# Performance work log

Measured on AMD Instinct MI355X. Metric: run time of the kernel, lower is better.

The kernel has to match this reference:

```python
import jax, jax.numpy as jnp
import numpy as np

E = 20000      # num edges
S = 64         # mul of 0e (scalar) channels
V = 32         # mul of 1o (vector) channels
FC_IN = 128    # radial basis length
HID = 64       # fc hidden width
INV_SQRT3 = 0.5773502691896258  # CG(1o x 1o -> 0e) = delta_ij / sqrt(3)


def setup_inputs() -> dict:
    key = jax.random.key(0)
    ks = jax.random.split(key, 16)
    n = jax.random.normal
    return {
        # edge features, layout [64 scalars | 32 vectors * 3 comps]
        "fea_in1": n(ks[0], (E, S + 3 * V), jnp.float32),
        "fea_in2": n(ks[1], (E, S + 3 * V), jnp.float32),
        "fea_weight": n(ks[2], (E, FC_IN), jnp.float32),
        # FullyConnectedTensorProduct internal weights (e3nn init: normal(0,1))
        "w_ss_s": n(ks[3], (S, S, S), jnp.float32),   # 0e x 0e -> 64x0e scalars
        "w_vv_s": n(ks[4], (V, V, S), jnp.float32),   # 1o x 1o -> 64x0e scalars
        "w_ss_g": n(ks[5], (S, S, V), jnp.float32),   # 0e x 0e -> 32x0e gates
        "w_vv_g": n(ks[6], (V, V, V), jnp.float32),   # 1o x 1o -> 32x0e gates
        "w_sv_v": n(ks[7], (S, V, V), jnp.float32),   # 0e x 1o -> 32x1o
        "w_vs_v": n(ks[8], (V, S, V), jnp.float32),   # 1o x 0e -> 32x1o
        # fc MLP: Linear(128,64) SiLU Linear(64,64) SiLU Linear(64,96)
        "fc_w1": n(ks[9], (FC_IN, HID), jnp.float32) / np.sqrt(FC_IN).astype(np.float32),
        "fc_b1": jnp.zeros((HID,), jnp.float32),
        "fc_w2": n(ks[10], (HID, HID), jnp.float32) / np.sqrt(HID).astype(np.float32),
        "fc_b2": jnp.zeros((HID,), jnp.float32),
        "fc_w3": n(ks[11], (HID, S + V), jnp.float32) / np.sqrt(HID).astype(np.float32),
        "fc_b3": jnp.zeros((S + V,), jnp.float32),
        "batch_edge": jnp.zeros((E,), jnp.int32),  # unused (norm='')
    }


def _equiconv(fea_in1, fea_in2, fea_weight,
              w_ss_s, w_vv_s, w_ss_g, w_vv_g, w_sv_v, w_vs_v,
              fc_w1, fc_b1, fc_w2, fc_b2, fc_w3, fc_b3):
    x1s, x1v = fea_in1[:, :S], fea_in1[:, S:].reshape(-1, V, 3)
    x2s, x2v = fea_in2[:, :S], fea_in2[:, S:].reshape(-1, V, 3)

    # path normalization: 1/sqrt(fan_in), fan_in = sum(mul1*mul2) over paths to output
    a_sc = 1.0 / np.sqrt(S * S + V * V).astype(np.float32)
    a_vec = 1.0 / np.sqrt(2 * S * V).astype(np.float32)

    # FullyConnectedTensorProduct (uvw connectivity)
    sc = a_sc * (jnp.einsum('eu,ev,uvw->ew', x1s, x2s, w_ss_s)
                 + INV_SQRT3 * jnp.einsum('eui,evi,uvw->ew', x1v, x2v, w_vv_s))
    g = a_sc * (jnp.einsum('eu,ev,uvw->ew', x1s, x2s, w_ss_g)
                + INV_SQRT3 * jnp.einsum('eui,evi,uvw->ew', x1v, x2v, w_vv_g))
    vec = a_vec * (jnp.einsum('eu,evi,uvw->ewi', x1s, x2v, w_sv_v)
                   + jnp.einsum('eui,ev,uvw->ewi', x1v, x2s, w_vs_v))

    # Gate: silu on scalars, sigmoid gates multiply the l>0 part
    sc = jax.nn.silu(sc)
    vec = vec * jax.nn.sigmoid(g)[:, :, None]

    # fc MLP producing per-channel elementwise conv weights
    h = jax.nn.silu(fea_weight @ fc_w1 + fc_b1)
    h = jax.nn.silu(h @ fc_w2 + fc_b2)
    w = h @ fc_w3 + fc_b3  # [E, S+V]

    # e3ElementWise: one scalar weight per channel (shared over m components)
    sc = sc * w[:, :S]
    vec = vec * w[:, S:, None]
    return jnp.concatenate([sc, vec.reshape(-1, 3 * V)], axis=-1)


def reference(fea_in1, fea_in2, fea_weight,
              w_ss_s, w_vv_s, w_ss_g, w_vv_g, w_sv_v, w_vs_v,
              fc_w1, fc_b1, fc_w2, fc_b2, fc_w3, fc_b3, batch_edge):
    del batch_edge  # only used by optional e3LayerNorm (norm='')
    return _equiconv(fea_in1, fea_in2, fea_weight,
                     w_ss_s, w_vv_s, w_ss_g, w_vv_g, w_sv_v, w_vs_v,
                     fc_w1, fc_b1, fc_w2, fc_b2, fc_w3, fc_b3)
```

## Files before the change

### kernel.cpp

```cpp
#include <hip/hip_runtime.h>


#define E_TOT 20000

typedef __attribute__((ext_vector_type(8))) short short8;
typedef __attribute__((ext_vector_type(4))) float f32x4;
typedef __attribute__((ext_vector_type(2))) __bf16 bf16x2;

#define FRAG_USH 512
#define HALF_USH 1536
#define CH_USH   3072
#define N_CH     52
#define NSLOT    3
#define STRIDE_W 159744
#define FC1_OFF  638976
#define FC2_OFF  647168
#define FC3_OFF  651264
#define WS_USH   657408

#define X1S_OFF  36864
#define X1V_OFF  41088
#define POOL_B   47360

__device__ __forceinline__ unsigned short f2b(float f){
  return __builtin_bit_cast(unsigned short, (__bf16)f);
}
__device__ __forceinline__ unsigned f2b2(float lo, float hi){
  bf16x2 t; t[0] = (__bf16)lo; t[1] = (__bf16)hi;
  return __builtin_bit_cast(unsigned, t);
}
__device__ __forceinline__ float b2f(unsigned short h){
  return __uint_as_float(((unsigned)h) << 16);
}
__device__ __forceinline__ float ulo(unsigned u){ return __uint_as_float(u << 16); }
__device__ __forceinline__ float uhi(unsigned u){ return __uint_as_float(u & 0xFFFF0000u); }
__device__ __forceinline__ f32x4 mfma16(short8 a, short8 b, f32x4 c){
  return __builtin_amdgcn_mfma_f32_16x16x32_bf16(a, b, c, 0, 0, 0);
}
union U8 { short8 v; unsigned u[4]; };
__device__ __forceinline__ float silu_f(float x){ return x/(1.f+__expf(-x)); }
__device__ __forceinline__ float sigm_f(float x){ return 1.f/(1.f+__expf(-x)); }

#define PACK8P(a, s, xp) { \
  a.u[0]=f2b2((s)*ulo((xp)[0]),(s)*uhi((xp)[0])); \
  a.u[1]=f2b2((s)*ulo((xp)[1]),(s)*uhi((xp)[1])); \
  a.u[2]=f2b2((s)*ulo((xp)[2]),(s)*uhi((xp)[2])); \
  a.u[3]=f2b2((s)*ulo((xp)[3]),(s)*uhi((xp)[3])); }

#define WVC(code) { __builtin_amdgcn_s_waitcnt(code); __builtin_amdgcn_sched_barrier(0xF); }
#define GUARD     { __builtin_amdgcn_s_waitcnt(0xC07F); __builtin_amdgcn_sched_barrier(0xF); }

__device__ __forceinline__ int fpos(int kl, int n16){
  return (kl>>3)*128 + n16*8 + (kl&7);
}

__global__ void prep_weights(const float* __restrict__ ss_s, const float* __restrict__ ss_g,
                             const float* __restrict__ vv_s, const float* __restrict__ vv_g,
                             const float* __restrict__ sv,   const float* __restrict__ vs,
                             const float* __restrict__ w1,   const float* __restrict__ w2,
                             const float* __restrict__ w3,   unsigned short* __restrict__ wsb)
{
  int g = blockIdx.x * 256 + threadIdx.x;
  if (g >= WS_USH/8) return;
  const int dest = g << 3;
  const float A_SC  = 0.013975424859373686f;
  const float A_VV  = (float)(0.013975424859373686 * 0.5773502691896258);
  const float A_VEC = 0.015625f;

  const float* src = nullptr;
  int stride = 0;
  float scale = 1.f;

  if (dest < FC1_OFF) {
    int wave = dest / STRIDE_W;
    int off  = dest - wave*STRIDE_W;
    int c    = off / CH_USH;
    int rem  = off - c*CH_USH;
    int t    = rem >> 9;
    int p    = rem & 511;
    int kl   = (p >> 7) << 3;
    int n16  = (p >> 3) & 15;
    if (c < 32) {
      int u = (wave<<4) + (c>>1);
      int v = ((c&1)<<5) + kl;
      if (t < 4) { src = ss_s + (u<<12)+(v<<6)+((t<<4)+n16);     stride = 64; }
      else       { src = ss_g + (u<<11)+(v<<5)+(((t-4)<<4)+n16); stride = 32; }
      scale = A_SC;
    } else if (c < 40) {
      int u = (wave<<3) + (c-32);
      int v = kl;
      if (t < 4) { src = vv_s + (u<<11)+(v<<6)+((t<<4)+n16);     stride = 64; }
      else       { src = vv_g + (u<<10)+(v<<5)+(((t-4)<<4)+n16); stride = 32; }
      scale = A_VV;
    } else if (c < 46) {
      int ul = (c-40)*3 + (t>>1);
      if (ul < 16) {
        int u = (wave<<4) + ul;
        src = sv + (u<<10)+(kl<<5)+(((t&1)<<4)+n16);
        stride = 32; scale = A_VEC;
      }
    } else {
      int cc = c - 46;
      int vh = cc/3, ch3 = cc - vh*3;
      int fseq = ch3*6 + t;
      if (fseq < 16) {
        int u = (wave<<3) + (fseq>>1);
        int v = (vh<<5) + kl;
        src = vs + (u<<11)+(v<<5)+(((fseq&1)<<4)+n16);
        stride = 32; scale = A_VEC;
      }
    }
  } else if (dest < FC2_OFF) {
    int off = dest - FC1_OFF;
    int fi = off >> 9, p = off & 511;
    int kl = (p>>7)<<3, n16 = (p>>3)&15;
    int k = ((fi>>2)<<5) + kl, n = ((fi&3)<<4) + n16;
    src = w1 + (k<<6) + n; stride = 64;
  } else if (dest < FC3_OFF) {
    int off = dest - FC2_OFF;
    int fi = off >> 9, p = off & 511;
    int kl = (p>>7)<<3, n16 = (p>>3)&15;
    int k = ((fi>>2)<<5) + kl, n = ((fi&3)<<4) + n16;
    src = w2 + (k<<6) + n; stride = 64;
  } else {
    int off = dest - FC3_OFF;
    int fi = off >> 9, p = off & 511;
    int kl = (p>>7)<<3, n16 = (p>>3)&15;
    int koff = fi/6, nhi = fi - koff*6;
    int k = (koff<<5) + kl, n = (nhi<<4) + n16;
    src = w3 + k*96 + n; stride = 96;
  }

  U8 a;
  if (src) {
    float v0 = scale * src[0*stride], v1 = scale * src[1*stride];
    float v2 = scale * src[2*stride], v3 = scale * src[3*stride];
    float v4 = scale * src[4*stride], v5 = scale * src[5*stride];
    float v6 = scale * src[6*stride], v7 = scale * src[7*stride];
    a.u[0] = f2b2(v0, v1); a.u[1] = f2b2(v2, v3);
    a.u[2] = f2b2(v4, v5); a.u[3] = f2b2(v6, v7);
  } else {
    a.u[0] = 0; a.u[1] = 0; a.u[2] = 0; a.u[3] = 0;
  }
  *(short8*)(wsb + dest) = a.v;
}

__global__ __launch_bounds__(256, 3)
void equiconv_main(const float* __restrict__ fea1,
                   const float* __restrict__ fea2,
                   const float* __restrict__ few,
                   const float* __restrict__ fb1,
                   const float* __restrict__ fb2,
                   const float* __restrict__ fb3,
                   const unsigned short* __restrict__ wsb,
                   float* __restrict__ out)
{
  __shared__ __align__(16) unsigned char pool[POOL_B];
  unsigned short* ring = (unsigned short*)pool;
  unsigned short* x1s_ = (unsigned short*)(pool + X1S_OFF);
  unsigned short* x1v_ = (unsigned short*)(pool + X1V_OFF);
  unsigned short* hb_  = (unsigned short*)(pool + X1S_OFF);
  float*          redf = (float*)pool;

  #define X1S(r, cc) x1s_[(r)*66 + (cc)]
  #define X1V(r, cc) x1v_[(r)*98 + (cc)]
  #define HB(w, r, cc) hb_[(((w)<<4) + (r))*72 + (cc)]

  const int tid  = threadIdx.x;
  const int lane = tid & 63, wv = tid >> 6;
  const int ln   = lane & 15, quad = lane >> 4, q8 = quad << 3;
  const int ebase = blockIdx.x << 5;

  for (int it = tid; it < 1280; it += 256){
    int row = it / 40, seg = it - row*40;
    float4 v1 = *(const float4*)(fea1 + (size_t)(ebase + row)*160 + seg*4);
    const float* p1 = (const float*)&v1;
    int c0 = seg*4;
    #pragma unroll
    for (int jj = 0; jj < 4; jj++){
      int col = c0 + jj;
      if (col < 64) X1S(row, col) = f2b(p1[jj]);
      else          X1V(row, col-64) = f2b(p1[jj]);
    }
  }
  __syncthreads();

  unsigned xep[2][4], xop[2][4], y0p[2][4], y1p[2][4], y2p[2][4];
  #pragma unroll
  for (int s = 0; s < 2; s++){
    const float* p = fea2 + (size_t)(ebase + s*16 + ln)*160;
    float4 a0 = *(const float4*)(p + q8);
    float4 a1 = *(const float4*)(p + q8 + 4);
    float4 b0 = *(const float4*)(p + 32 + q8);
    float4 b1 = *(const float4*)(p + 36 + q8);
    xep[s][0]=f2b2(a0.x,a0.y); xep[s][1]=f2b2(a0.z,a0.w);
    xep[s][2]=f2b2(a1.x,a1.y); xep[s][3]=f2b2(a1.z,a1.w);
    xop[s][0]=f2b2(b0.x,b0.y); xop[s][1]=f2b2(b0.z,b0.w);
    xop[s][2]=f2b2(b1.x,b1.y); xop[s][3]=f2b2(b1.z,b1.w);
    const float* py = p + 64 + q8*3;
    float yb[24];
    #pragma unroll
    for (int t = 0; t < 12; t++){
      float2 f2v = *(const float2*)(py + 2*t);
      yb[2*t] = f2v.x; yb[2*t+1] = f2v.y;
    }
    #pragma unroll
    for (int q = 0; q < 4; q++){
      y0p[s][q] = f2b2(yb[6*q+0], yb[6*q+3]);
      y1p[s][q] = f2b2(yb[6*q+1], yb[6*q+4]);
      y2p[s][q] = f2b2(yb[6*q+2], yb[6*q+5]);
    }
  }

  const unsigned short* gstream = wsb + (size_t)wv*STRIDE_W;
  const int rbase = wv*NSLOT*HALF_USH;
  auto issue_half = [&](int h){
    const unsigned short* g = gstream + h*HALF_USH + lane*8;
    unsigned short* l = &ring[rbase + (h%NSLOT)*HALF_USH];
    #pragma unroll
    for (int q = 0; q < 3; q++)
      __builtin_amdgcn_global_load_lds(
        (const __attribute__((address_space(1))) unsigned int*)(g + q*FRAG_USH),
        (__attribute__((address_space(3))) unsigned int*)(l + q*FRAG_USH),
        16, 0, 0);
  };
  issue_half(0); issue_half(1); issue_half(2);

  const int r0 = ln, r1 = 16 + ln;
  const f32x4 z4 = {0.f,0.f,0.f,0.f};
  f32x4 accS[2][6] = {{z4,z4,z4,z4,z4,z4},{z4,z4,z4,z4,z4,z4}};
  f32x4 accV[2][3][2] = {{{z4,z4},{z4,z4},{z4,z4}},{{z4,z4},{z4,z4},{z4,z4}}};

  #define READCH(cc, bb, WA, IA, WB, IB) { \
    const int h0_ = 2*(cc); \
    WVC(WA); \
    { const unsigned short* pA_ = &ring[rbase + (h0_%NSLOT)*HALF_USH + lane*8]; \
      bb[0] = *(const short8*)(pA_); \
      bb[1] = *(const short8*)(pA_ + FRAG_USH); \
      bb[2] = *(const short8*)(pA_ + 2*FRAG_USH); } \
    if (IA) { GUARD; issue_half(h0_ + 3); } \
    WVC(WB); \
    { const unsigned short* pB_ = &ring[rbase + ((h0_+1)%NSLOT)*HALF_USH + lane*8]; \
      bb[3] = *(const short8*)(pB_); \
      bb[4] = *(const short8*)(pB_ + FRAG_USH); \
      bb[5] = *(const short8*)(pB_ + 2*FRAG_USH); } \
    if (IB) { GUARD; issue_half(h0_ + 4); } }

  #pragma unroll 2
  for (int c = 0; c < 32; c++){
    int u = (wv<<4) + (c>>1);
    float s0 = b2f(X1S(r0, u));
    float s1 = b2f(X1S(r1, u));
    U8 a0, a1;
    if (c & 1){ PACK8P(a0, s0, xop[0]); PACK8P(a1, s1, xop[1]); }
    else      { PACK8P(a0, s0, xep[0]); PACK8P(a1, s1, xep[1]); }
    short8 bb[6];
    READCH(c, bb, 0x0F76, 1, 0x0F76, 1);
    #pragma unroll
    for (int t = 0; t < 6; t++){
      accS[0][t] = mfma16(a0.v, bb[t], accS[0][t]);
      accS[1][t] = mfma16(a1.v, bb[t], accS[1][t]);
    }
  }
  #pragma unroll 1
  for (int k8 = 0; k8 < 8; k8++){
    int c = 32 + k8, u = (wv<<3) + k8;
    U8 a[2];
    #pragma unroll
    for (int s = 0; s < 2; s++){
      int rr = s ? r1 : r0;
      float c0 = b2f(X1V(rr, u*3+0));
      float c1 = b2f(X1V(rr, u*3+1));
      float c2 = b2f(X1V(rr, u*3+2));
      #pragma unroll
      for (int q = 0; q < 4; q++){
        float lo = c0*ulo(y0p[s][q]) + c1*ulo(y1p[s][q]) + c2*ulo(y2p[s][q]);
        float hi = c0*uhi(y0p[s][q]) + c1*uhi(y1p[s][q]) + c2*uhi(y2p[s][q]);
        a[s].u[q] = f2b2(lo, hi);
      }
    }
    short8 bb[6];
    READCH(c, bb, 0x0F76, 1, 0x0F76, 1);
    #pragma unroll
    for (int t = 0; t < 6; t++){
      accS[0][t] = mfma16(a[0].v, bb[t], accS[0][t]);
      accS[1][t] = mfma16(a[1].v, bb[t], accS[1][t]);
    }
  }
  #pragma unroll 1
  for (int ch = 0; ch < 6; ch++){
    int c = 40 + ch;
    short8 bb[6];
    READCH(c, bb, 0x0F76, 1, 0x0F76, 1);
    #pragma unroll
    for (int uu = 0; uu < 3; uu++){
      int ui = ch*3 + uu;
      if (ui < 16){
        int u = (wv<<4) + ui;
        float s0 = b2f(X1S(r0, u));
        float s1 = b2f(X1S(r1, u));
        U8 a[2][3];
        PACK8P(a[0][0], s0, y0p[0]); PACK8P(a[0][1], s0, y1p[0]); PACK8P(a[0][2], s0, y2p[0]);
        PACK8P(a[1][0], s1, y0p[1]); PACK8P(a[1][1], s1, y1p[1]); PACK8P(a[1][2], s1, y2p[1]);
        #pragma unroll
        for (int t = 0; t < 2; t++){
          short8 b8 = bb[uu*2 + t];
          #pragma unroll
          for (int s = 0; s < 2; s++)
            #pragma unroll
            for (int i = 0; i < 3; i++)
              accV[s][i][t] = mfma16(a[s][i].v, b8, accV[s][i][t]);
        }
      }
    }
  }
  #define VSBODY(pcv, bb) { \
    const int p_ = (pcv)/3, ch_ = (pcv) - p_*3; \
    _Pragma("unroll") \
    for (int uu = 0; uu < 3; uu++){ \
      int ui = ch_*3 + uu; \
      if (ui < 8){ \
        int u = (wv<<3) + ui; \
        U8 a[2][3]; \
        _Pragma("unroll") \
        for (int s = 0; s < 2; s++){ \
          int rr = s ? r1 : r0; \
          float c0 = b2f(X1V(rr, u*3+0)); \
          float c1 = b2f(X1V(rr, u*3+1)); \
          float c2 = b2f(X1V(rr, u*3+2)); \
          const unsigned* xx = p_ ? xop[s] : xep[s]; \
          PACK8P(a[s][0], c0, xx); PACK8P(a[s][1], c1, xx); PACK8P(a[s][2], c2, xx); \
        } \
        _Pragma("unroll") \
        for (int t = 0; t < 2; t++){ \
          short8 b8 = bb[uu*2 + t]; \
          _Pragma("unroll") \
          for (int s = 0; s < 2; s++) \
            _Pragma("unroll") \
            for (int i = 0; i < 3; i++) \
              accV[s][i][t] = mfma16(a[s][i].v, b8, accV[s][i][t]); \
        } \
      } \
    } }

  #pragma unroll 1
  for (int pc = 0; pc < 4; pc++){
    short8 bb[6];
    READCH(46+pc, bb, 0x0F76, 1, 0x0F76, 1);
    VSBODY(pc, bb);
  }
  {
    short8 bb[6];
    READCH(50, bb, 0x0F76, 1, 0x0F76, 0);
    VSBODY(4, bb);
  }
  {
    short8 bb[6];
    READCH(51, bb, 0x0F73, 0, 0x0F70, 0);
    VSBODY(5, bb);
  }

  f32x4 T0[12], T1[12];
  #pragma unroll
  for (int t = 0; t < 6; t++){ T0[t] = accS[0][t]; T1[t] = accS[1][t]; }
  #pragma unroll
  for (int t = 0; t < 2; t++)
    #pragma unroll
    for (int i = 0; i < 3; i++){
      T0[6+3*t+i] = accV[0][i][t]; T1[6+3*t+i] = accV[1][i][t];
    }

  #define PUT12(base, T) { _Pragma("unroll") for (int j=0;j<12;j++) \
    *(f32x4*)(redf + ((base)+j)*320 + ln*20 + (quad<<2)) = T[j]; }
  #define ADD12(base, T) { _Pragma("unroll") for (int j=0;j<12;j++) \
    T[j] += *(const f32x4*)(redf + ((base)+j)*320 + ln*20 + (quad<<2)); }

  __syncthreads();
  if (wv==1) PUT12(0, T0);  if (wv==2) PUT12(12, T1);
  __syncthreads();
  if (wv==0) ADD12(0, T0);  if (wv==3) ADD12(12, T1);
  __syncthreads();
  if (wv==2) PUT12(0, T0);  if (wv==1) PUT12(12, T1);
  __syncthreads();
  if (wv==0) ADD12(0, T0);  if (wv==3) ADD12(12, T1);
  __syncthreads();
  if (wv==3) PUT12(0, T0);  if (wv==0) PUT12(12, T1);
  __syncthreads();
  if (wv==0) ADD12(0, T0);  if (wv==3) ADD12(12, T1);

  if (wv == 1 || wv == 2) return;
  const int s = (wv == 0) ? 0 : 1;
  f32x4* P = (wv == 0) ? T0 : T1;

  f32x4 accF[4] = {z4,z4,z4,z4};
  {
    const float* fwp = few + (size_t)(ebase + s*16 + ln)*128;
    const short8* B = (const short8*)(wsb + FC1_OFF);
    #pragma unroll
    for (int c = 0; c < 4; c++){
      float4 fa  = *(const float4*)(fwp + c*32 + q8);
      float4 fbv = *(const float4*)(fwp + c*32 + q8 + 4);
      U8 a;
      a.u[0]=f2b2(fa.x,fa.y);   a.u[1]=f2b2(fa.z,fa.w);
      a.u[2]=f2b2(fbv.x,fbv.y); a.u[3]=f2b2(fbv.z,fbv.w);
      #pragma unroll
      for (int t = 0; t < 4; t++) accF[t] = mfma16(a.v, B[(c*4+t)*64 + lane], accF[t]);
    }
  }
  #pragma unroll
  for (int t = 0; t < 4; t++){
    float bb = fb1[(t<<4)+ln];
    #pragma unroll
    for (int r = 0; r < 4; r++)
      HB(wv, (quad<<2)+r, (t<<4)+ln) = f2b(silu_f(accF[t][r] + bb));
  }
  f32x4 acc2[4] = {z4,z4,z4,z4};
  {
    const short8* B = (const short8*)(wsb + FC2_OFF);
    #pragma unroll
    for (int c = 0; c < 2; c++){
      uint4 hq = *(const uint4*)&HB(wv, ln, c*32 + q8);
      U8 a; a.u[0]=hq.x; a.u[1]=hq.y; a.u[2]=hq.z; a.u[3]=hq.w;
      #pragma unroll
      for (int t = 0; t < 4; t++) acc2[t] = mfma16(a.v, B[(c*4+t)*64 + lane], acc2[t]);
    }
  }
  #pragma unroll
  for (int t = 0; t < 4; t++){
    float bb = fb2[(t<<4)+ln];
    #pragma unroll
    for (int r = 0; r < 4; r++)
      HB(wv, (quad<<2)+r, (t<<4)+ln) = f2b(silu_f(acc2[t][r] + bb));
  }
  f32x4 acc3[6] = {z4,z4,z4,z4,z4,z4};
  {
    const short8* B = (const short8*)(wsb + FC3_OFF);
    #pragma unroll
    for (int c = 0; c < 2; c++){
      uint4 hq = *(const uint4*)&HB(wv, ln, c*32 + q8);
      U8 a; a.u[0]=hq.x; a.u[1]=hq.y; a.u[2]=hq.z; a.u[3]=hq.w;
      #pragma unroll
      for (int t = 0; t < 6; t++) acc3[t] = mfma16(a.v, B[(c*6+t)*64 + lane], acc3[t]);
    }
  }

  #pragma unroll
  for (int r = 0; r < 4; r++){
    int eg = ebase + s*16 + (quad<<2) + r;
    float* op = out + (size_t)eg*160;
    #pragma unroll
    for (int t = 0; t < 4; t++)
      op[(t<<4)+ln] = silu_f(P[t][r]) * (acc3[t][r] + fb3[(t<<4)+ln]);
    #pragma unroll
    for (int tp = 0; tp < 2; tp++){
      int wc = (tp<<4) + ln;
      float f = sigm_f(P[4+tp][r]) * (acc3[4+tp][r] + fb3[64+wc]);
      op[64 + wc*3 + 0] = P[6+3*tp+0][r] * f;
      op[64 + wc*3 + 1] = P[6+3*tp+1][r] * f;
      op[64 + wc*3 + 2] = P[6+3*tp+2][r] * f;
    }
  }
}

extern "C" void kernel_launch(void* const* d_in, const int* in_sizes, int n_in,
                              void* d_out, int out_size, void* d_ws, size_t ws_size,
                              hipStream_t stream) {
  (void)in_sizes; (void)n_in; (void)out_size; (void)ws_size;
  unsigned short* wsb = (unsigned short*)d_ws;

  prep_weights<<<(WS_USH/8 + 255)/256, 256, 0, stream>>>(
      (const float*)d_in[3], (const float*)d_in[5],
      (const float*)d_in[4], (const float*)d_in[6],
      (const float*)d_in[7], (const float*)d_in[8],
      (const float*)d_in[9], (const float*)d_in[11], (const float*)d_in[13],
      wsb);

  equiconv_main<<<E_TOT/32, 256, 0, stream>>>(
      (const float*)d_in[0], (const float*)d_in[1], (const float*)d_in[2],
      (const float*)d_in[10], (const float*)d_in[12], (const float*)d_in[14],
      (const unsigned short*)wsb, (float*)d_out);
}
```

Measured before the change: 191.2 us.

## Replace LDS ring of async weight loads with register double-buffered global loads

The weight stream was staged through a 3-slot LDS ring filled by global_load_lds, with hand-placed waitcnts. It is now read directly from global memory into two register buffers, ping-ponging so chunk c+1 loads while chunk c is consumed by MFMAs. This removes the LDS ring, its wait/guard stalls and extra LDS reads, and shrinks shared memory. The cost is more VGPR pressure, so launch bounds drop from 3 to 2 blocks per CU, which risks lower occupancy and less latency hiding.

```diff
diff --git a/kernel.cpp b/kernel.cpp
--- a/kernel.cpp
+++ b/kernel.cpp
@@ -8,19 +8,17 @@
 typedef __attribute__((ext_vector_type(2))) __bf16 bf16x2;
 
 #define FRAG_USH 512
-#define HALF_USH 1536
 #define CH_USH   3072
 #define N_CH     52
-#define NSLOT    3
 #define STRIDE_W 159744
 #define FC1_OFF  638976
 #define FC2_OFF  647168
 #define FC3_OFF  651264
 #define WS_USH   657408
 
-#define X1S_OFF  36864
-#define X1V_OFF  41088
-#define POOL_B   47360
+#define X1S_OFF  30720
+#define X1V_OFF  34944
+#define POOL_B   41216
 
 __device__ __forceinline__ unsigned short f2b(float f){
   return __builtin_bit_cast(unsigned short, (__bf16)f);
@@ -46,9 +44,6 @@
   a.u[1]=f2b2((s)*ulo((xp)[1]),(s)*uhi((xp)[1])); \
   a.u[2]=f2b2((s)*ulo((xp)[2]),(s)*uhi((xp)[2])); \
   a.u[3]=f2b2((s)*ulo((xp)[3]),(s)*uhi((xp)[3])); }
-
-#define WVC(code) { __builtin_amdgcn_s_waitcnt(code); __builtin_amdgcn_sched_barrier(0xF); }
-#define GUARD     { __builtin_amdgcn_s_waitcnt(0xC07F); __builtin_amdgcn_sched_barrier(0xF); }
 
 __device__ __forceinline__ int fpos(int kl, int n16){
   return (kl>>3)*128 + n16*8 + (kl&7);
@@ -145,7 +140,7 @@
   *(short8*)(wsb + dest) = a.v;
 }
 
-__global__ __launch_bounds__(256, 3)
+__global__ __launch_bounds__(256, 2)
 void equiconv_main(const float* __restrict__ fea1,
                    const float* __restrict__ fea2,
                    const float* __restrict__ few,
@@ -156,11 +151,10 @@
                    float* __restrict__ out)
 {
   __shared__ __align__(16) unsigned char pool[POOL_B];
-  unsigned short* ring = (unsigned short*)pool;
+  float*          redf = (float*)pool;
   unsigned short* x1s_ = (unsigned short*)(pool + X1S_OFF);
   unsigned short* x1v_ = (unsigned short*)(pool + X1V_OFF);
   unsigned short* hb_  = (unsigned short*)(pool + X1S_OFF);
-  float*          redf = (float*)pool;
 
   #define X1S(r, cc) x1s_[(r)*66 + (cc)]
   #define X1V(r, cc) x1v_[(r)*98 + (cc)]
@@ -212,109 +206,109 @@
     }
   }
 
-  const unsigned short* gstream = wsb + (size_t)wv*STRIDE_W;
-  const int rbase = wv*NSLOT*HALF_USH;
-  auto issue_half = [&](int h){
-    const unsigned short* g = gstream + h*HALF_USH + lane*8;
-    unsigned short* l = &ring[rbase + (h%NSLOT)*HALF_USH];
-    #pragma unroll
-    for (int q = 0; q < 3; q++)
-      __builtin_amdgcn_global_load_lds(
-        (const __attribute__((address_space(1))) unsigned int*)(g + q*FRAG_USH),
-        (__attribute__((address_space(3))) unsigned int*)(l + q*FRAG_USH),
-        16, 0, 0);
+  const unsigned short* gstream = wsb + (size_t)wv*STRIDE_W + lane*8;
+  auto LD = [&](int c, short8* buf){
+    const unsigned short* g = gstream + c*CH_USH;
+    #pragma unroll
+    for (int t = 0; t < 6; t++) buf[t] = *(const short8*)(g + t*FRAG_USH);
   };
-  issue_half(0); issue_half(1); issue_half(2);
 
   const int r0 = ln, r1 = 16 + ln;
   const f32x4 z4 = {0.f,0.f,0.f,0.f};
   f32x4 accS[2][6] = {{z4,z4,z4,z4,z4,z4},{z4,z4,z4,z4,z4,z4}};
   f32x4 accV[2][3][2] = {{{z4,z4},{z4,z4},{z4,z4}},{{z4,z4},{z4,z4},{z4,z4}}};
 
-  #define READCH(cc, bb, WA, IA, WB, IB) { \
-    const int h0_ = 2*(cc); \
-    WVC(WA); \
-    { const unsigned short* pA_ = &ring[rbase + (h0_%NSLOT)*HALF_USH + lane*8]; \
-      bb[0] = *(const short8*)(pA_); \
-      bb[1] = *(const short8*)(pA_ + FRAG_USH); \
-      bb[2] = *(const short8*)(pA_ + 2*FRAG_USH); } \
-    if (IA) { GUARD; issue_half(h0_ + 3); } \
-    WVC(WB); \
-    { const unsigned short* pB_ = &ring[rbase + ((h0_+1)%NSLOT)*HALF_USH + lane*8]; \
-      bb[3] = *(const short8*)(pB_); \
-      bb[4] = *(const short8*)(pB_ + FRAG_USH); \
-      bb[5] = *(const short8*)(pB_ + 2*FRAG_USH); } \
-    if (IB) { GUARD; issue_half(h0_ + 4); } }
-
-  #pragma unroll 2
-  for (int c = 0; c < 32; c++){
-    int u = (wv<<4) + (c>>1);
+  short8 bA[6], bB[6];
+  LD(0, bA);
+
+  #pragma unroll 1
+  for (int cc = 0; cc < 16; cc++){
+    int u = (wv<<4) + cc;
     float s0 = b2f(X1S(r0, u));
     float s1 = b2f(X1S(r1, u));
-    U8 a0, a1;
-    if (c & 1){ PACK8P(a0, s0, xop[0]); PACK8P(a1, s1, xop[1]); }
-    else      { PACK8P(a0, s0, xep[0]); PACK8P(a1, s1, xep[1]); }
-    short8 bb[6];
-    READCH(c, bb, 0x0F76, 1, 0x0F76, 1);
-    #pragma unroll
-    for (int t = 0; t < 6; t++){
-      accS[0][t] = mfma16(a0.v, bb[t], accS[0][t]);
-      accS[1][t] = mfma16(a1.v, bb[t], accS[1][t]);
-    }
-  }
+    {
+      LD(2*cc+1, bB);
+      U8 a0, a1;
+      PACK8P(a0, s0, xep[0]); PACK8P(a1, s1, xep[1]);
+      #pragma unroll
+      for (int t = 0; t < 6; t++){
+        accS[0][t] = mfma16(a0.v, bA[t], accS[0][t]);
+        accS[1][t] = mfma16(a1.v, bA[t], accS[1][t]);
+      }
+    }
+    {
+      LD(2*cc+2, bA);
+      U8 a0, a1;
+      PACK8P(a0, s0, xop[0]); PACK8P(a1, s1, xop[1]);
+      #pragma unroll
+      for (int t = 0; t < 6; t++){
+        accS[0][t] = mfma16(a0.v, bB[t], accS[0][t]);
+        accS[1][t] = mfma16(a1.v, bB[t], accS[1][t]);
+      }
+    }
+  }
+  #define VVA(uV, s, aa) { \
+    int rr = (s) ? r1 : r0; \
+    float c0 = b2f(X1V(rr, (uV)*3+0)); \
+    float c1 = b2f(X1V(rr, (uV)*3+1)); \
+    float c2 = b2f(X1V(rr, (uV)*3+2)); \
+    _Pragma("unroll") \
+    for (int q = 0; q < 4; q++){ \
+      float lo = c0*ulo(y0p[s][q]) + c1*ulo(y1p[s][q]) + c2*ulo(y2p[s][q]); \
+      float hi = c0*uhi(y0p[s][q]) + c1*uhi(y1p[s][q]) + c2*uhi(y2p[s][q]); \
+      aa.u[q] = f2b2(lo, hi); \
+    } }
   #pragma unroll 1
-  for (int k8 = 0; k8 < 8; k8++){
-    int c = 32 + k8, u = (wv<<3) + k8;
-    U8 a[2];
-    #pragma unroll
-    for (int s = 0; s < 2; s++){
-      int rr = s ? r1 : r0;
-      float c0 = b2f(X1V(rr, u*3+0));
-      float c1 = b2f(X1V(rr, u*3+1));
-      float c2 = b2f(X1V(rr, u*3+2));
-      #pragma unroll
-      for (int q = 0; q < 4; q++){
-        float lo = c0*ulo(y0p[s][q]) + c1*ulo(y1p[s][q]) + c2*ulo(y2p[s][q]);
-        float hi = c0*uhi(y0p[s][q]) + c1*uhi(y1p[s][q]) + c2*uhi(y2p[s][q]);
-        a[s].u[q] = f2b2(lo, hi);
-      }
-    }
-    short8 bb[6];
-    READCH(c, bb, 0x0F76, 1, 0x0F76, 1);
-    #pragma unroll
-    for (int t = 0; t < 6; t++){
-      accS[0][t] = mfma16(a[0].v, bb[t], accS[0][t]);
-      accS[1][t] = mfma16(a[1].v, bb[t], accS[1][t]);
-    }
-  }
+  for (int k8 = 0; k8 < 8; k8 += 2){
+    {
+      LD(33+k8, bB);
+      int u = (wv<<3) + k8;
+      U8 a0, a1; VVA(u, 0, a0); VVA(u, 1, a1);
+      #pragma unroll
+      for (int t = 0; t < 6; t++){
+        accS[0][t] = mfma16(a0.v, bA[t], accS[0][t]);
+        accS[1][t] = mfma16(a1.v, bA[t], accS[1][t]);
+      }
+    }
+    {
+      LD(34+k8, bA);
+      int u = (wv<<3) + k8 + 1;
+      U8 a0, a1; VVA(u, 0, a0); VVA(u, 1, a1);
+      #pragma unroll
+      for (int t = 0; t < 6; t++){
+        accS[0][t] = mfma16(a0.v, bB[t], accS[0][t]);
+        accS[1][t] = mfma16(a1.v, bB[t], accS[1][t]);
+      }
+    }
+  }
+  #define SVBODY(chv, buf) { \
+    _Pragma("unroll") \
+    for (int uu = 0; uu < 3; uu++){ \
+      int ui = (chv)*3 + uu; \
+      if (ui < 16){ \
+        int u = (wv<<4) + ui; \
+        float s0 = b2f(X1S(r0, u)); \
+        float s1 = b2f(X1S(r1, u)); \
+        U8 a[2][3]; \
+        PACK8P(a[0][0], s0, y0p[0]); PACK8P(a[0][1], s0, y1p[0]); PACK8P(a[0][2], s0, y2p[0]); \
+        PACK8P(a[1][0], s1, y0p[1]); PACK8P(a[1][1], s1, y1p[1]); PACK8P(a[1][2], s1, y2p[1]); \
+        _Pragma("unroll") \
+        for (int t = 0; t < 2; t++){ \
+          short8 b8 = buf[uu*2 + t]; \
+          _Pragma("unroll") \
+          for (int s = 0; s < 2; s++) \
+            _Pragma("unroll") \
+            for (int i = 0; i < 3; i++) \
+              accV[s][i][t] = mfma16(a[s][i].v, b8, accV[s][i][t]); \
+        } \
+      } \
+    } }
   #pragma unroll 1
-  for (int ch = 0; ch < 6; ch++){
-    int c = 40 + ch;
-    short8 bb[6];
-    READCH(c, bb, 0x0F76, 1, 0x0F76, 1);
-    #pragma unroll
-    for (int uu = 0; uu < 3; uu++){
-      int ui = ch*3 + uu;
-      if (ui < 16){
-        int u = (wv<<4) + ui;
-        float s0 = b2f(X1S(r0, u));
-        float s1 = b2f(X1S(r1, u));
-        U8 a[2][3];
-        PACK8P(a[0][0], s0, y0p[0]); PACK8P(a[0][1], s0, y1p[0]); PACK8P(a[0][2], s0, y2p[0]);
-        PACK8P(a[1][0], s1, y0p[1]); PACK8P(a[1][1], s1, y1p[1]); PACK8P(a[1][2], s1, y2p[1]);
-        #pragma unroll
-        for (int t = 0; t < 2; t++){
-          short8 b8 = bb[uu*2 + t];
-          #pragma unroll
-          for (int s = 0; s < 2; s++)
-            #pragma unroll
-            for (int i = 0; i < 3; i++)
-              accV[s][i][t] = mfma16(a[s][i].v, b8, accV[s][i][t]);
-        }
-      }
-    }
-  }
-  #define VSBODY(pcv, bb) { \
+  for (int ch = 0; ch < 6; ch += 2){
+    { LD(41+ch, bB); SVBODY(ch, bA); }
+    { LD(42+ch, bA); SVBODY(ch+1, bB); }
+  }
+  #define VSBODY(pcv, buf) { \
     const int p_ = (pcv)/3, ch_ = (pcv) - p_*3; \
     _Pragma("unroll") \
     for (int uu = 0; uu < 3; uu++){ \
@@ -333,7 +327,7 @@
         } \
         _Pragma("unroll") \
         for (int t = 0; t < 2; t++){ \
-          short8 b8 = bb[uu*2 + t]; \
+          short8 b8 = buf[uu*2 + t]; \
           _Pragma("unroll") \
           for (int s = 0; s < 2; s++) \
             _Pragma("unroll") \
@@ -342,23 +336,12 @@
         } \
       } \
     } }
-
-  #pragma unroll 1
-  for (int pc = 0; pc < 4; pc++){
-    short8 bb[6];
-    READCH(46+pc, bb, 0x0F76, 1, 0x0F76, 1);
-    VSBODY(pc, bb);
-  }
-  {
-    short8 bb[6];
-    READCH(50, bb, 0x0F76, 1, 0x0F76, 0);
-    VSBODY(4, bb);
-  }
-  {
-    short8 bb[6];
-    READCH(51, bb, 0x0F73, 0, 0x0F70, 0);
-    VSBODY(5, bb);
-  }
+  { LD(47, bB); VSBODY(0, bA); }
+  { LD(48, bA); VSBODY(1, bB); }
+  { LD(49, bB); VSBODY(2, bA); }
+  { LD(50, bA); VSBODY(3, bB); }
+  { LD(51, bB); VSBODY(4, bA); }
+  { VSBODY(5, bB); }
 
   f32x4 T0[12], T1[12];
   #pragma unroll
```

Measured after the change: 182.4 us. 4.6% less time.
